# Optimization experiments

Hardware: AMD Instinct MI355X
Metric: run time of the kernel (lower is better)

Reference implementation:

```python
import jax, jax.numpy as jnp
from jax import lax
import numpy as np

MAX_SEQ_LEN = 8192
B, S, D = 8, 8192, 1024
LN_EPS = 1e-5

# ---------- static lattice structure (pure Python, replicates original incl. quirks) ----------

def _gen_spine(max_len):
    s = [0, 2, 4]
    while True:
        nxt = 2 * s[-1] + 2 * s[-2] + 2 * s[-3]
        if nxt >= max_len:
            break
        s.append(nxt)
    return s

def _imm_anc(spine, pos):
    if pos in spine:
        i = spine.index(pos)
        if i >= 3:
            return [spine[i - 1], spine[i - 2], spine[i - 3]]
    return []

def _analyze(spine, pos):
    # BFS over ancestors; NOTE: levels[level+1] is OVERWRITTEN per popped node,
    # exactly as in the original torch code.
    visited = {pos}
    levels = {0: [pos]}
    queue = [(pos, 0)]
    while queue:
        cur, lvl = queue.pop(0)
        if lvl >= 9:
            break
        newl = []
        for a in _imm_anc(spine, cur):
            if a not in visited and a >= 0:
                visited.add(a)
                newl.append(a)
                queue.append((a, lvl + 1))
        if newl:
            levels[lvl + 1] = list(newl)
    max_depth = max(levels.keys())
    pc = {pos: 1}
    for lvl in sorted(levels.keys(), reverse=True):
        for node in levels[lvl]:
            if node == pos:
                continue
            if lvl == max_depth:
                pc[node] = 1
                continue
            c = 0
            for ch in levels.get(lvl + 1, []):
                if node in _imm_anc(spine, ch):
                    c += pc.get(ch, 0)
            if lvl != 0:
                pc[node] = c
    pc.pop(pos, None)
    return levels, pc

def _structures(seq_len):
    spine = _gen_spine(MAX_SEQ_LEN)
    out = []
    for pos in spine:
        if pos >= seq_len or pos < 3:
            continue
        levels, pc = _analyze(spine, pos)
        anc, cnt = [], []
        for lvl in levels:  # dict insertion order == level order, as in torch
            if lvl > 0:
                for a in levels[lvl]:
                    if a < seq_len:
                        anc.append(a)
                        cnt.append(float(pc.get(a, 1)))
        if anc:
            out.append((pos, np.array(anc, np.int32), np.array(cnt, np.float32)))
    return out

# ---------- neural pieces ----------

def _gru_last(seq, w_ih, w_hh, b_ih, b_hh):
    # seq: [B, K, D]; single-layer batch_first GRU, h0 = 0; returns last hidden [B, D]
    d = w_hh.shape[1]
    def step(h, xt):
        gi = xt @ w_ih.T + b_ih   # [B, 3D]
        gh = h @ w_hh.T + b_hh
        i_r, i_z, i_n = jnp.split(gi, 3, axis=-1)
        h_r, h_z, h_n = jnp.split(gh, 3, axis=-1)
        r = jax.nn.sigmoid(i_r + h_r)
        z = jax.nn.sigmoid(i_z + h_z)
        n = jnp.tanh(i_n + r * h_n)
        return (1.0 - z) * n + z * h, None
    h0 = jnp.zeros((seq.shape[0], d), seq.dtype)
    hT, _ = lax.scan(step, h0, jnp.swapaxes(seq, 0, 1))
    return hT

def reference(x, pw_w1, pw_b1, pw_w2, pw_b2, msg_w, msg_b, ln_g, ln_b,
              gru_w_ih, gru_w_hh, gru_b_ih, gru_b_hh, gate_w, gate_b):
    structs = _structures(x.shape[1])
    out = x
    for pos, anc, cnt in structs:
        # path weights: Linear(1,64)->ReLU->Linear(64,1)->Softplus  on counts [K,1]
        c = jnp.asarray(cnt)[:, None]
        w = jax.nn.softplus(jnp.squeeze(jax.nn.relu(c @ pw_w1.T + pw_b1) @ pw_w2.T + pw_b2))  # [K]
        h_anc = x[:, anc, :]                         # [B, K, D] gather
        h_cur = x[:, pos, :]                         # [B, D]
        pair = jnp.concatenate([h_anc, jnp.broadcast_to(h_cur[:, None, :], h_anc.shape)], axis=-1)
        m = pair @ msg_w.T + msg_b                   # [B, K, D]
        mu = m.mean(-1, keepdims=True)
        var = ((m - mu) ** 2).mean(-1, keepdims=True)
        m = (m - mu) / jnp.sqrt(var + LN_EPS) * ln_g + ln_b
        m = jax.nn.gelu(m, approximate=False)
        m = m * w[None, :, None]                     # path-weighted messages
        agg = _gru_last(m, gru_w_ih, gru_w_hh, gru_b_ih, gru_b_hh)  # [B, D]
        g = jax.nn.sigmoid(jnp.concatenate([agg, h_cur], axis=-1) @ gate_w.T + gate_b)
        out = out.at[:, pos, :].set(g * agg + (1.0 - g) * h_cur)
    return out

def setup_inputs() -> dict:
    key = jax.random.key(0)
    ks = jax.random.split(key, 8)
    def n(k, shape, s=0.02):
        return jax.random.normal(k, shape, jnp.float32) * s
    return {
        "x": jax.random.normal(ks[0], (B, S, D), jnp.float32),
        "pw_w1": n(ks[1], (64, 1), 0.5), "pw_b1": jnp.zeros((64,), jnp.float32),
        "pw_w2": n(ks[2], (1, 64), 0.5), "pw_b2": jnp.zeros((1,), jnp.float32),
        "msg_w": n(ks[3], (D, 2 * D)), "msg_b": jnp.zeros((D,), jnp.float32),
        "ln_g": jnp.ones((D,), jnp.float32), "ln_b": jnp.zeros((D,), jnp.float32),
        "gru_w_ih": n(ks[4], (3 * D, D)), "gru_w_hh": n(ks[5], (3 * D, D)),
        "gru_b_ih": jnp.zeros((3 * D,), jnp.float32), "gru_b_hh": jnp.zeros((3 * D,), jnp.float32),
        "gate_w": n(ks[6], (D, 2 * D)), "gate_b": jnp.zeros((D,), jnp.float32),
    }
```

## Files before the change

### kernel.cpp

```cpp
#include <hip/hip_runtime.h>
#include <math.h>
#include <string.h>

#define SEQ 8192
#define DIM 1024
#define NBATCH 8

typedef float vf4 __attribute__((ext_vector_type(4)));

struct SDesc {
  int n, Tmax, totalRows;
  int pos[8], A[8], rowbase[8];
  int anc[8][8];
  float cnt[8][8];
  int nu;
  int upos[16];
  int up_of_s[8];
  int s_of_rr[32], a_of_rr[32], ua_of_rr[32];
};

static SDesc build_structs() {
  SDesc H{};
  int spine[24];
  int ns = 3; spine[0] = 0; spine[1] = 2; spine[2] = 4;
  for (;;) {
    long nxt = 2L * (spine[ns-1] + spine[ns-2] + spine[ns-3]);
    if (nxt >= SEQ) break;
    spine[ns++] = (int)nxt;
  }
  int rb = 0;
  for (int i = 0; i < ns; ++i) {
    int pos = spine[i];
    if (pos < 3) continue;
    bool visited[24] = {false};
    int levels[12][8]; int lcnt[12];
    for (int l = 0; l < 12; ++l) lcnt[l] = 0;
    levels[0][0] = i; lcnt[0] = 1; visited[i] = true;
    int qidx[64], qlvl[64], qh = 0, qt = 0;
    qidx[qt] = i; qlvl[qt] = 0; qt++;
    int maxd = 0;
    while (qh < qt) {
      int cur = qidx[qh], lvl = qlvl[qh]; qh++;
      if (lvl >= 9) break;
      int newl[8], nn = 0;
      if (cur >= 3) {
        for (int d = 1; d <= 3; ++d) {
          int a = cur - d;
          if (!visited[a]) { visited[a] = true; newl[nn++] = a; qidx[qt] = a; qlvl[qt] = lvl + 1; qt++; }
        }
      }
      if (nn) {
        lcnt[lvl+1] = nn;
        for (int k = 0; k < nn; ++k) levels[lvl+1][k] = newl[k];
        if (lvl + 1 > maxd) maxd = lvl + 1;
      }
    }
    float pcv[24]; bool pcs[24];
    for (int k = 0; k < 24; ++k) { pcv[k] = 0.f; pcs[k] = false; }
    pcv[i] = 1.f; pcs[i] = true;
    for (int lvl = maxd; lvl >= 0; --lvl) {
      for (int nidx = 0; nidx < lcnt[lvl]; ++nidx) {
        int node = levels[lvl][nidx];
        if (node == i) continue;
        if (lvl == maxd) { pcv[node] = 1.f; pcs[node] = true; continue; }
        float c = 0.f;
        for (int cidx = 0; cidx < lcnt[lvl+1]; ++cidx) {
          int ch = levels[lvl+1][cidx];
          if (ch >= 3 && node >= ch - 3 && node <= ch - 1) c += pcs[ch] ? pcv[ch] : 0.f;
        }
        if (lvl != 0) { pcv[node] = c; pcs[node] = true; }
      }
    }
    int A = 0;
    int sidx = H.n;
    for (int lvl = 1; lvl <= maxd; ++lvl) {
      for (int nidx = 0; nidx < lcnt[lvl]; ++nidx) {
        int node = levels[lvl][nidx];
        H.anc[sidx][A] = spine[node];
        H.cnt[sidx][A] = pcs[node] ? pcv[node] : 1.f;
        A++;
      }
    }
    if (A == 0) continue;
    H.pos[sidx] = pos; H.A[sidx] = A; H.rowbase[sidx] = rb; rb += A;
    H.n++;
  }
  H.totalRows = rb;
  H.Tmax = 0;
  for (int s = 0; s < H.n; ++s) if (H.A[s] > H.Tmax) H.Tmax = H.A[s];
  int vals[128], nv = 0;
  for (int s = 0; s < H.n; ++s) {
    vals[nv++] = H.pos[s];
    for (int a = 0; a < H.A[s]; ++a) vals[nv++] = H.anc[s][a];
  }
  H.nu = 0;
  for (int i = 0; i < nv; ++i) {
    bool seen = false;
    for (int u = 0; u < H.nu; ++u) if (H.upos[u] == vals[i]) { seen = true; break; }
    if (!seen) H.upos[H.nu++] = vals[i];
  }
  for (int i = 0; i < H.nu; ++i)
    for (int j2 = i + 1; j2 < H.nu; ++j2)
      if (H.upos[j2] < H.upos[i]) { int t = H.upos[i]; H.upos[i] = H.upos[j2]; H.upos[j2] = t; }
  auto uidx = [&](int v) { for (int u = 0; u < H.nu; ++u) if (H.upos[u] == v) return u; return 0; };
  for (int s = 0; s < H.n; ++s) {
    H.up_of_s[s] = uidx(H.pos[s]);
    for (int a = 0; a < H.A[s]; ++a) {
      int rr = H.rowbase[s] + a;
      H.s_of_rr[rr] = s; H.a_of_rr[rr] = a; H.ua_of_rr[rr] = uidx(H.anc[s][a]);
    }
  }
  return H;
}


__device__ __forceinline__ void do_copy(const vf4* __restrict__ src, vf4* __restrict__ dst,
                                        int q, int nc, int start4, int n4) {
  for (int i = q * 256 + threadIdx.x; i < n4; i += nc * 256) {
    vf4 v = __builtin_nontemporal_load(&src[start4 + i]);
    __builtin_nontemporal_store(v, &dst[start4 + i]);
  }
}

__device__ __forceinline__ float wred(float v) {
  #pragma unroll
  for (int off = 32; off; off >>= 1) v += __shfl_xor(v, off);
  return v;
}

__device__ __forceinline__ float dot4(vf4 a, vf4 b) {
  return a.x * b.x + a.y * b.y + a.z * b.z + a.w * b.w;
}


__global__ void k_prepzero(SDesc sd, const float* __restrict__ w1, const float* __restrict__ b1,
                           const float* __restrict__ w2, const float* __restrict__ b2,
                           float* __restrict__ wout, vf4* __restrict__ hz, int nzero4,
                           int NC, const vf4* __restrict__ csrc, vf4* __restrict__ cdst,
                           int cstart, int cn) {
  int p = blockIdx.x;
  if (p >= 57) { do_copy(csrc, cdst, p - 57, NC, cstart, cn); return; }
  if (p == 0) {
    int t = threadIdx.x;
    int s = t >> 3, a = t & 7;
    if (t < 64 && s < sd.n && a < sd.A[s]) {
      float v = sd.cnt[s][a];
      float acc = 0.f;
      for (int i = 0; i < 64; ++i) {
        float h = v * w1[i] + b1[i];
        if (h > 0.f) acc += h * w2[i];
      }
      float o = acc + b2[0];
      float sp = (o > 0.f) ? (o + log1pf(expf(-o))) : log1pf(expf(o));
      wout[s * 8 + a] = sp;
    }
  } else {
    int base = (p - 1) * 512 + threadIdx.x;
    if (base < nzero4)       hz[base]       = (vf4)(0.f);
    if (base + 256 < nzero4) hz[base + 256] = (vf4)(0.f);
  }
}

__global__ __launch_bounds__(256, 2) void k_T(SDesc sd, const float* __restrict__ x,
    const float* __restrict__ msg_w, float* __restrict__ T,
    int NC, const vf4* __restrict__ csrc, vf4* __restrict__ cdst, int cstart, int cn) {
  int p = blockIdx.x;
  const int NMAIN = 1280;
  if (p >= NMAIN) { do_copy(csrc, cdst, p - NMAIN, NC, cstart, cn); return; }
  int q = p % 128, rt = p / 128;
  int jt = (q & 7) * 16 + (q >> 3);

  int wave = threadIdx.x >> 6, lane = threadIdx.x & 63;
  int jc0 = jt * 16 + wave * 4;
  const vf4* mw4 = (const vf4*)msg_w;
  size_t b0 = (size_t)((jc0 + 0) & 1023) * 512 + (((jc0 + 0) >> 10) << 8);
  size_t b1 = (size_t)((jc0 + 1) & 1023) * 512 + (((jc0 + 1) >> 10) << 8);
  size_t b2 = (size_t)((jc0 + 2) & 1023) * 512 + (((jc0 + 2) >> 10) << 8);
  size_t b3 = (size_t)((jc0 + 3) & 1023) * 512 + (((jc0 + 3) >> 10) << 8);
  vf4 w0[4], w1[4], w2[4], w3[4];
  #pragma unroll
  for (int c = 0; c < 4; ++c) {
    w0[c] = mw4[b0 + c * 64 + lane];
    w1[c] = mw4[b1 + c * 64 + lane];
    w2[c] = mw4[b2 + c * 64 + lane];
    w3[c] = mw4[b3 + c * 64 + lane];
  }
  const vf4* x4 = (const vf4*)x;
  #pragma unroll 2
  for (int r = 0; r < 8; ++r) {
    int row = rt * 8 + r; int u = row >> 3, b = row & 7;
    size_t rb4 = ((size_t)b * SEQ + sd.upos[u]) * 256;
    vf4 a0 = x4[rb4 + 0 * 64 + lane], a1 = x4[rb4 + 1 * 64 + lane];
    vf4 a2 = x4[rb4 + 2 * 64 + lane], a3 = x4[rb4 + 3 * 64 + lane];
    float s0 = dot4(w0[0], a0) + dot4(w0[1], a1) + dot4(w0[2], a2) + dot4(w0[3], a3);
    float s1 = dot4(w1[0], a0) + dot4(w1[1], a1) + dot4(w1[2], a2) + dot4(w1[3], a3);
    float s2 = dot4(w2[0], a0) + dot4(w2[1], a1) + dot4(w2[2], a2) + dot4(w2[3], a3);
    float s3 = dot4(w3[0], a0) + dot4(w3[1], a1) + dot4(w3[2], a2) + dot4(w3[3], a3);
    s0 = wred(s0); s1 = wred(s1); s2 = wred(s2); s3 = wred(s3);
    if (lane == 0) {
      float* tp = T + (size_t)row * 2048 + jc0;
      tp[0] = s0; tp[1] = s1; tp[2] = s2; tp[3] = s3;
    }
  }
}

__global__ __launch_bounds__(256) void k_ln(SDesc sd, const float* __restrict__ ln_g,
    const float* __restrict__ ln_b, const float* __restrict__ msg_b,
    const float* __restrict__ wsc, const float* __restrict__ T, float* __restrict__ mseq,
    int M, int NC, const vf4* __restrict__ csrc, vf4* __restrict__ cdst, int cstart, int cn) {
  int p = blockIdx.x;
  if (p >= M) { do_copy(csrc, cdst, p - M, NC, cstart, cn); return; }
  int rr = p >> 3, b = p & 7;
  int s = sd.s_of_rr[rr], a = sd.a_of_rr[rr];
  int ua = sd.ua_of_rr[rr], up = sd.up_of_s[s];
  float wmul = wsc[s * 8 + a];
  const vf4* Tl = (const vf4*)(T + ((size_t)ua * 8 + b) * 2048);
  const vf4* Tr = (const vf4*)(T + ((size_t)up * 8 + b) * 2048 + 1024);
  const vf4* mb = (const vf4*)msg_b;
  int t = threadIdx.x;
  vf4 vl = Tl[t], vr = Tr[t], vb = mb[t];
  vf4 v; v.x = vl.x + vr.x + vb.x; v.y = vl.y + vr.y + vb.y;
  v.z = vl.z + vr.z + vb.z; v.w = vl.w + vr.w + vb.w;
  float sum = v.x + v.y + v.z + v.w;
  float sq  = v.x * v.x + v.y * v.y + v.z * v.z + v.w * v.w;
  #pragma unroll
  for (int off = 32; off; off >>= 1) { sum += __shfl_xor(sum, off); sq += __shfl_xor(sq, off); }
  __shared__ float s1[4], s2[4];
  int wave = t >> 6, lane = t & 63;
  if (lane == 0) { s1[wave] = sum; s2[wave] = sq; }
  __syncthreads();
  sum = s1[0] + s1[1] + s1[2] + s1[3];
  sq  = s2[0] + s2[1] + s2[2] + s2[3];
  float mu  = sum * (1.f / 1024.f);
  float var = sq * (1.f / 1024.f) - mu * mu;
  float inv = rsqrtf(var + 1e-5f);
  vf4 g4 = ((const vf4*)ln_g)[t];
  vf4 b4 = ((const vf4*)ln_b)[t];
  float o[4]  = {v.x, v.y, v.z, v.w};
  float gg[4] = {g4.x, g4.y, g4.z, g4.w};
  float bb[4] = {b4.x, b4.y, b4.z, b4.w};
  #pragma unroll
  for (int i = 0; i < 4; ++i) {
    float u = (o[i] - mu) * inv * gg[i] + bb[i];
    float ge = 0.5f * u * (1.f + erff(u * 0.70710678118654752f));
    o[i] = ge * wmul;
  }
  vf4 ov; ov.x = o[0]; ov.y = o[1]; ov.z = o[2]; ov.w = o[3];
  ((vf4*)(mseq + (size_t)p * DIM))[t] = ov;
}

__global__ __launch_bounds__(256, 2) void k_gi(const float* __restrict__ mseq,
    const float* __restrict__ wih, const float* __restrict__ bih, float* __restrict__ gi,
    int NC, const vf4* __restrict__ csrc, vf4* __restrict__ cdst, int cstart, int cn) {
  int p = blockIdx.x;
  const int NMAIN = 2880;
  if (p >= NMAIN) { do_copy(csrc, cdst, p - NMAIN, NC, cstart, cn); return; }
  int q = p % 192, rt = p / 192;
  int jt = (q & 7) * 24 + (q >> 3);

  int wave = threadIdx.x >> 6, lane = threadIdx.x & 63;
  int j0 = jt * 16 + wave * 4;
  const vf4* wp4 = (const vf4*)wih;
  vf4 w0[4], w1[4], w2[4], w3[4];
  #pragma unroll
  for (int c = 0; c < 4; ++c) {
    w0[c] = wp4[(size_t)(j0 + 0) * 256 + c * 64 + lane];
    w1[c] = wp4[(size_t)(j0 + 1) * 256 + c * 64 + lane];
    w2[c] = wp4[(size_t)(j0 + 2) * 256 + c * 64 + lane];
    w3[c] = wp4[(size_t)(j0 + 3) * 256 + c * 64 + lane];
  }
  const vf4* m4 = (const vf4*)mseq;
  #pragma unroll 2
  for (int r = 0; r < 16; ++r) {
    int row = rt * 16 + r;
    size_t rb4 = (size_t)row * 256;
    vf4 a0 = m4[rb4 + 0 * 64 + lane], a1 = m4[rb4 + 1 * 64 + lane];
    vf4 a2 = m4[rb4 + 2 * 64 + lane], a3 = m4[rb4 + 3 * 64 + lane];
    float s0 = dot4(w0[0], a0) + dot4(w0[1], a1) + dot4(w0[2], a2) + dot4(w0[3], a3);
    float s1 = dot4(w1[0], a0) + dot4(w1[1], a1) + dot4(w1[2], a2) + dot4(w1[3], a3);
    float s2 = dot4(w2[0], a0) + dot4(w2[1], a1) + dot4(w2[2], a2) + dot4(w2[3], a3);
    float s3 = dot4(w3[0], a0) + dot4(w3[1], a1) + dot4(w3[2], a2) + dot4(w3[3], a3);
    s0 = wred(s0); s1 = wred(s1); s2 = wred(s2); s3 = wred(s3);
    if (lane == 0) {
      float* gp = gi + (size_t)row * 3072 + j0;
      gp[0] = s0 + bih[j0 + 0]; gp[1] = s1 + bih[j0 + 1];
      gp[2] = s2 + bih[j0 + 2]; gp[3] = s3 + bih[j0 + 3];
    }
  }
}

__global__ __launch_bounds__(256, 2) void k_step(SDesc sd, int t,
    const float* __restrict__ whh, const float* __restrict__ bhh,
    const float* __restrict__ gi, const float* __restrict__ hold, float* __restrict__ hnew,
    int NC, const vf4* __restrict__ csrc, vf4* __restrict__ cdst, int cstart, int cn) {
  int p = blockIdx.x;
  const int NMAIN = 7 * 256;
  if (p >= NMAIN) { do_copy(csrc, cdst, p - NMAIN, NC, cstart, cn); return; }
  int q = p & 255, s = p >> 8;
  int jt = (q & 7) * 32 + (q >> 3);
  int t0 = sd.Tmax - sd.A[s];
  if (t < t0) return;
  int a = t - t0;

  int wave = threadIdx.x >> 6, lane = threadIdx.x & 63;
  int j = jt * 4 + wave;
  const vf4* wp4 = (const vf4*)whh;
  vf4 wr[4], wz[4], wn[4];
  #pragma unroll
  for (int c = 0; c < 4; ++c) {
    wr[c] = wp4[(size_t)j * 256 + c * 64 + lane];
    wz[c] = wp4[(size_t)(1024 + j) * 256 + c * 64 + lane];
    wn[c] = wp4[(size_t)(2048 + j) * 256 + c * 64 + lane];
  }
  const vf4* h4 = (const vf4*)hold;
  #pragma unroll 2
  for (int r = 0; r < 8; ++r) {
    int srow = s * 8 + r;
    size_t rb4 = (size_t)srow * 256;
    vf4 a0 = h4[rb4 + 0 * 64 + lane], a1 = h4[rb4 + 1 * 64 + lane];
    vf4 a2 = h4[rb4 + 2 * 64 + lane], a3 = h4[rb4 + 3 * 64 + lane];
    float ar = dot4(wr[0], a0) + dot4(wr[1], a1) + dot4(wr[2], a2) + dot4(wr[3], a3);
    float az = dot4(wz[0], a0) + dot4(wz[1], a1) + dot4(wz[2], a2) + dot4(wz[3], a3);
    float an = dot4(wn[0], a0) + dot4(wn[1], a1) + dot4(wn[2], a2) + dot4(wn[3], a3);
    ar = wred(ar); az = wred(az); an = wred(an);
    if (lane == 0) {
      int girow = (sd.rowbase[s] + a) * 8 + r;
      const float* gp = gi + (size_t)girow * 3072;
      float hr = ar + bhh[j];
      float hz = az + bhh[1024 + j];
      float hn = an + bhh[2048 + j];
      float rg = 1.f / (1.f + expf(-(gp[j] + hr)));
      float zg = 1.f / (1.f + expf(-(gp[1024 + j] + hz)));
      float ng = tanhf(gp[2048 + j] + rg * hn);
      float ho = hold[(size_t)srow * DIM + j];
      hnew[(size_t)srow * DIM + j] = (1.f - zg) * ng + zg * ho;
    }
  }
}

__global__ __launch_bounds__(256, 2) void k_gate(SDesc sd, const float* __restrict__ x,
    const float* __restrict__ gw, const float* __restrict__ gb,
    const float* __restrict__ hfin, float* __restrict__ out) {
  int p = blockIdx.x;
  int q = p % 128, rt = p / 128;
  int jt = (q & 7) * 16 + (q >> 3);

  int wave = threadIdx.x >> 6, lane = threadIdx.x & 63;
  int j0 = jt * 8 + wave * 2;
  const vf4* g4p = (const vf4*)gw;
  vf4 wL0[4], wR0[4], wL1[4], wR1[4];
  #pragma unroll
  for (int c = 0; c < 4; ++c) {
    wL0[c] = g4p[(size_t)(j0 + 0) * 512 + c * 64 + lane];
    wR0[c] = g4p[(size_t)(j0 + 0) * 512 + 256 + c * 64 + lane];
    wL1[c] = g4p[(size_t)(j0 + 1) * 512 + c * 64 + lane];
    wR1[c] = g4p[(size_t)(j0 + 1) * 512 + 256 + c * 64 + lane];
  }
  const vf4* h4 = (const vf4*)hfin;
  const vf4* x4 = (const vf4*)x;
  #pragma unroll 2
  for (int r = 0; r < 8; ++r) {
    int row = rt * 8 + r; int s = row >> 3, b = row & 7;
    size_t ab4 = (size_t)row * 256;
    size_t xb4 = ((size_t)b * SEQ + sd.pos[s]) * 256;
    vf4 a0 = h4[ab4 + 0 * 64 + lane], a1 = h4[ab4 + 1 * 64 + lane];
    vf4 a2 = h4[ab4 + 2 * 64 + lane], a3 = h4[ab4 + 3 * 64 + lane];
    vf4 x0 = x4[xb4 + 0 * 64 + lane], x1 = x4[xb4 + 1 * 64 + lane];
    vf4 x2 = x4[xb4 + 2 * 64 + lane], x3 = x4[xb4 + 3 * 64 + lane];
    float s0 = dot4(wL0[0], a0) + dot4(wL0[1], a1) + dot4(wL0[2], a2) + dot4(wL0[3], a3)
             + dot4(wR0[0], x0) + dot4(wR0[1], x1) + dot4(wR0[2], x2) + dot4(wR0[3], x3);
    float s1 = dot4(wL1[0], a0) + dot4(wL1[1], a1) + dot4(wL1[2], a2) + dot4(wL1[3], a3)
             + dot4(wR1[0], x0) + dot4(wR1[1], x1) + dot4(wR1[2], x2) + dot4(wR1[3], x3);
    s0 = wred(s0); s1 = wred(s1);
    if (lane == 0) {
      #pragma unroll
      for (int jj = 0; jj < 2; ++jj) {
        int j = j0 + jj;
        float sv = jj ? s1 : s0;
        float g = 1.f / (1.f + expf(-(sv + gb[j])));
        float agg = hfin[(size_t)row * DIM + j];
        float hc  = x[((size_t)b * SEQ + sd.pos[s]) * DIM + j];
        out[((size_t)b * SEQ + sd.pos[s]) * DIM + j] = g * agg + (1.f - g) * hc;
      }
    }
  }
}


extern "C" void kernel_launch(void* const* d_in, const int* in_sizes, int n_in,
                              void* d_out, int out_size, void* d_ws, size_t ws_size,
                              hipStream_t stream) {
  const float* x      = (const float*)d_in[0];
  const float* pw_w1  = (const float*)d_in[1];
  const float* pw_b1  = (const float*)d_in[2];
  const float* pw_w2  = (const float*)d_in[3];
  const float* pw_b2  = (const float*)d_in[4];
  const float* msg_w  = (const float*)d_in[5];
  const float* msg_b  = (const float*)d_in[6];
  const float* ln_g   = (const float*)d_in[7];
  const float* ln_b   = (const float*)d_in[8];
  const float* w_ih   = (const float*)d_in[9];
  const float* w_hh   = (const float*)d_in[10];
  const float* b_ih   = (const float*)d_in[11];
  const float* b_hh   = (const float*)d_in[12];
  const float* gate_w = (const float*)d_in[13];
  const float* gate_b = (const float*)d_in[14];
  float* out = (float*)d_out;
  float* ws  = (float*)d_ws;

  SDesc sd = build_structs();
  const int M = sd.totalRows * 8;

  float* wout = ws;
  float* T    = wout + 64;
  float* mseq = T + (size_t)sd.nu * 8 * 2048;
  float* gi   = mseq + (size_t)240 * DIM;
  float* h0   = gi + (size_t)240 * 3072;
  float* h1   = h0 + (size_t)sd.n * 8 * DIM;

  const vf4* x4 = (const vf4*)x;
  vf4* out4 = (vf4*)out;
  const int TOTAL4 = (NBATCH * SEQ * DIM) / 4;
  const int c_big = 2200000;
  const int rem = TOTAL4 - 4 * c_big;
  const int c_step = rem / 5;

  int nzero4 = (2 * sd.n * 8 * DIM) / 4;

  int off = 0;
  k_prepzero<<<57 + 1024, 256, 0, stream>>>(sd, pw_w1, pw_b1, pw_w2, pw_b2, wout,
                                            (vf4*)h0, nzero4, 1024, x4, out4, off, c_big);
  off += c_big;

  k_T<<<1280 + 1024, 256, 0, stream>>>(sd, x, msg_w, T, 1024, x4, out4, off, c_big);
  off += c_big;

  k_ln<<<M + 1024, 256, 0, stream>>>(sd, ln_g, ln_b, msg_b, wout, T, mseq,
                                     M, 1024, x4, out4, off, c_big);
  off += c_big;

  k_gi<<<2880 + 1024, 256, 0, stream>>>(mseq, w_ih, b_ih, gi, 1024, x4, out4, off, c_big);
  off += c_big;

  for (int t = 0; t < sd.Tmax; ++t) {
    const float* hr = (t & 1) ? h1 : h0;
    float*       hw = (t & 1) ? h0 : h1;
    int cnt = (t == sd.Tmax - 1) ? (TOTAL4 - off) : c_step;
    k_step<<<7 * 256 + 768, 256, 0, stream>>>(sd, t, w_hh, b_hh, gi, hr, hw,
                                              768, x4, out4, off, cnt);
    off += cnt;
  }
  const float* hfin = (sd.Tmax & 1) ? h1 : h0;

  k_gate<<<128 * 7, 256, 0, stream>>>(sd, x, gate_w, gate_b, hfin, out);

  (void)in_sizes; (void)n_in; (void)out_size; (void)ws_size;
}
```

Measured before the change: 301.5 us.

## Skip hidden-state zeroing by special-casing first GRU step, fuse prep into k_T

Removes the separate prep/zero kernel. The pathweight MLP now runs as an extra block inside k_T, and the first GRU step (a==0) computes its result directly with h=0, so there is no zeroed h buffer to read and no W_hh matvec for that step. The step kernel hoists the gi and bias loads out of the lane-0 epilogue, occupancy hints rise from 2 to 4 blocks per CU, and the background copy is split into new per-kernel chunk sizes with more copy blocks. This saves a launch and some memory traffic, but higher occupancy may force register spills in the weight-resident kernels.

```diff
diff --git a/kernel.cpp b/kernel.cpp
--- a/kernel.cpp
+++ b/kernel.cpp
@@ -133,14 +133,14 @@
 }
 
 
-__global__ void k_prepzero(SDesc sd, const float* __restrict__ w1, const float* __restrict__ b1,
-                           const float* __restrict__ w2, const float* __restrict__ b2,
-                           float* __restrict__ wout, vf4* __restrict__ hz, int nzero4,
-                           int NC, const vf4* __restrict__ csrc, vf4* __restrict__ cdst,
-                           int cstart, int cn) {
+__global__ __launch_bounds__(256, 4) void k_T(SDesc sd, const float* __restrict__ x,
+    const float* __restrict__ msg_w, float* __restrict__ T,
+    const float* __restrict__ w1, const float* __restrict__ b1,
+    const float* __restrict__ w2, const float* __restrict__ b2, float* __restrict__ wout,
+    int NC, const vf4* __restrict__ csrc, vf4* __restrict__ cdst, int cstart, int cn) {
   int p = blockIdx.x;
-  if (p >= 57) { do_copy(csrc, cdst, p - 57, NC, cstart, cn); return; }
-  if (p == 0) {
+  const int NMAIN = 1280;
+  if (p == NMAIN) {
     int t = threadIdx.x;
     int s = t >> 3, a = t & 7;
     if (t < 64 && s < sd.n && a < sd.A[s]) {
@@ -154,19 +154,9 @@
       float sp = (o > 0.f) ? (o + log1pf(expf(-o))) : log1pf(expf(o));
       wout[s * 8 + a] = sp;
     }
-  } else {
-    int base = (p - 1) * 512 + threadIdx.x;
-    if (base < nzero4)       hz[base]       = (vf4)(0.f);
-    if (base + 256 < nzero4) hz[base + 256] = (vf4)(0.f);
-  }
-}
-
-__global__ __launch_bounds__(256, 2) void k_T(SDesc sd, const float* __restrict__ x,
-    const float* __restrict__ msg_w, float* __restrict__ T,
-    int NC, const vf4* __restrict__ csrc, vf4* __restrict__ cdst, int cstart, int cn) {
-  int p = blockIdx.x;
-  const int NMAIN = 1280;
-  if (p >= NMAIN) { do_copy(csrc, cdst, p - NMAIN, NC, cstart, cn); return; }
+    return;
+  }
+  if (p > NMAIN) { do_copy(csrc, cdst, p - NMAIN - 1, NC, cstart, cn); return; }
   int q = p % 128, rt = p / 128;
   int jt = (q & 7) * 16 + (q >> 3);
 
@@ -174,16 +164,16 @@
   int jc0 = jt * 16 + wave * 4;
   const vf4* mw4 = (const vf4*)msg_w;
   size_t b0 = (size_t)((jc0 + 0) & 1023) * 512 + (((jc0 + 0) >> 10) << 8);
-  size_t b1 = (size_t)((jc0 + 1) & 1023) * 512 + (((jc0 + 1) >> 10) << 8);
-  size_t b2 = (size_t)((jc0 + 2) & 1023) * 512 + (((jc0 + 2) >> 10) << 8);
+  size_t b1_ = (size_t)((jc0 + 1) & 1023) * 512 + (((jc0 + 1) >> 10) << 8);
+  size_t b2_ = (size_t)((jc0 + 2) & 1023) * 512 + (((jc0 + 2) >> 10) << 8);
   size_t b3 = (size_t)((jc0 + 3) & 1023) * 512 + (((jc0 + 3) >> 10) << 8);
-  vf4 w0[4], w1[4], w2[4], w3[4];
+  vf4 w0[4], w1v[4], w2v[4], w3[4];
   #pragma unroll
   for (int c = 0; c < 4; ++c) {
-    w0[c] = mw4[b0 + c * 64 + lane];
-    w1[c] = mw4[b1 + c * 64 + lane];
-    w2[c] = mw4[b2 + c * 64 + lane];
-    w3[c] = mw4[b3 + c * 64 + lane];
+    w0[c]  = mw4[b0  + c * 64 + lane];
+    w1v[c] = mw4[b1_ + c * 64 + lane];
+    w2v[c] = mw4[b2_ + c * 64 + lane];
+    w3[c]  = mw4[b3  + c * 64 + lane];
   }
   const vf4* x4 = (const vf4*)x;
   #pragma unroll 2
@@ -192,10 +182,10 @@
     size_t rb4 = ((size_t)b * SEQ + sd.upos[u]) * 256;
     vf4 a0 = x4[rb4 + 0 * 64 + lane], a1 = x4[rb4 + 1 * 64 + lane];
     vf4 a2 = x4[rb4 + 2 * 64 + lane], a3 = x4[rb4 + 3 * 64 + lane];
-    float s0 = dot4(w0[0], a0) + dot4(w0[1], a1) + dot4(w0[2], a2) + dot4(w0[3], a3);
-    float s1 = dot4(w1[0], a0) + dot4(w1[1], a1) + dot4(w1[2], a2) + dot4(w1[3], a3);
-    float s2 = dot4(w2[0], a0) + dot4(w2[1], a1) + dot4(w2[2], a2) + dot4(w2[3], a3);
-    float s3 = dot4(w3[0], a0) + dot4(w3[1], a1) + dot4(w3[2], a2) + dot4(w3[3], a3);
+    float s0 = dot4(w0[0],  a0) + dot4(w0[1],  a1) + dot4(w0[2],  a2) + dot4(w0[3],  a3);
+    float s1 = dot4(w1v[0], a0) + dot4(w1v[1], a1) + dot4(w1v[2], a2) + dot4(w1v[3], a3);
+    float s2 = dot4(w2v[0], a0) + dot4(w2v[1], a1) + dot4(w2v[2], a2) + dot4(w2v[3], a3);
+    float s3 = dot4(w3[0],  a0) + dot4(w3[1],  a1) + dot4(w3[2],  a2) + dot4(w3[3],  a3);
     s0 = wred(s0); s1 = wred(s1); s2 = wred(s2); s3 = wred(s3);
     if (lane == 0) {
       float* tp = T + (size_t)row * 2048 + jc0;
@@ -249,7 +239,7 @@
   ((vf4*)(mseq + (size_t)p * DIM))[t] = ov;
 }
 
-__global__ __launch_bounds__(256, 2) void k_gi(const float* __restrict__ mseq,
+__global__ __launch_bounds__(256, 4) void k_gi(const float* __restrict__ mseq,
     const float* __restrict__ wih, const float* __restrict__ bih, float* __restrict__ gi,
     int NC, const vf4* __restrict__ csrc, vf4* __restrict__ cdst, int cstart, int cn) {
   int p = blockIdx.x;
@@ -289,7 +279,7 @@
   }
 }
 
-__global__ __launch_bounds__(256, 2) void k_step(SDesc sd, int t,
+__global__ __launch_bounds__(256, 4) void k_step(SDesc sd, int t,
     const float* __restrict__ whh, const float* __restrict__ bhh,
     const float* __restrict__ gi, const float* __restrict__ hold, float* __restrict__ hnew,
     int NC, const vf4* __restrict__ csrc, vf4* __restrict__ cdst, int cstart, int cn) {
@@ -304,6 +294,20 @@
 
   int wave = threadIdx.x >> 6, lane = threadIdx.x & 63;
   int j = jt * 4 + wave;
+  int girow0 = (sd.rowbase[s] + a) * 8;
+
+  if (a == 0) {
+    if (lane < 8) {
+      int r = lane;
+      const float* gp = gi + (size_t)(girow0 + r) * 3072;
+      float rg = 1.f / (1.f + expf(-(gp[j] + bhh[j])));
+      float zg = 1.f / (1.f + expf(-(gp[1024 + j] + bhh[1024 + j])));
+      float ng = tanhf(gp[2048 + j] + rg * bhh[2048 + j]);
+      hnew[(size_t)(s * 8 + r) * DIM + j] = (1.f - zg) * ng;
+    }
+    return;
+  }
+
   const vf4* wp4 = (const vf4*)whh;
   vf4 wr[4], wz[4], wn[4];
   #pragma unroll
@@ -312,11 +316,14 @@
     wz[c] = wp4[(size_t)(1024 + j) * 256 + c * 64 + lane];
     wn[c] = wp4[(size_t)(2048 + j) * 256 + c * 64 + lane];
   }
+  float bj_r = bhh[j], bj_z = bhh[1024 + j], bj_n = bhh[2048 + j];
   const vf4* h4 = (const vf4*)hold;
   #pragma unroll 2
   for (int r = 0; r < 8; ++r) {
     int srow = s * 8 + r;
     size_t rb4 = (size_t)srow * 256;
+    const float* gp = gi + (size_t)(girow0 + r) * 3072;
+    float gir = gp[j], giz = gp[1024 + j], gin = gp[2048 + j];
     vf4 a0 = h4[rb4 + 0 * 64 + lane], a1 = h4[rb4 + 1 * 64 + lane];
     vf4 a2 = h4[rb4 + 2 * 64 + lane], a3 = h4[rb4 + 3 * 64 + lane];
     float ar = dot4(wr[0], a0) + dot4(wr[1], a1) + dot4(wr[2], a2) + dot4(wr[3], a3);
@@ -324,21 +331,16 @@
     float an = dot4(wn[0], a0) + dot4(wn[1], a1) + dot4(wn[2], a2) + dot4(wn[3], a3);
     ar = wred(ar); az = wred(az); an = wred(an);
     if (lane == 0) {
-      int girow = (sd.rowbase[s] + a) * 8 + r;
-      const float* gp = gi + (size_t)girow * 3072;
-      float hr = ar + bhh[j];
-      float hz = az + bhh[1024 + j];
-      float hn = an + bhh[2048 + j];
-      float rg = 1.f / (1.f + expf(-(gp[j] + hr)));
-      float zg = 1.f / (1.f + expf(-(gp[1024 + j] + hz)));
-      float ng = tanhf(gp[2048 + j] + rg * hn);
+      float rg = 1.f / (1.f + expf(-(gir + ar + bj_r)));
+      float zg = 1.f / (1.f + expf(-(giz + az + bj_z)));
+      float ng = tanhf(gin + rg * (an + bj_n));
       float ho = hold[(size_t)srow * DIM + j];
       hnew[(size_t)srow * DIM + j] = (1.f - zg) * ng + zg * ho;
     }
   }
 }
 
-__global__ __launch_bounds__(256, 2) void k_gate(SDesc sd, const float* __restrict__ x,
+__global__ __launch_bounds__(256, 4) void k_gate(SDesc sd, const float* __restrict__ x,
     const float* __restrict__ gw, const float* __restrict__ gb,
     const float* __restrict__ hfin, float* __restrict__ out) {
   int p = blockIdx.x;
@@ -421,33 +423,32 @@
   const vf4* x4 = (const vf4*)x;
   vf4* out4 = (vf4*)out;
   const int TOTAL4 = (NBATCH * SEQ * DIM) / 4;
-  const int c_big = 2200000;
-  const int rem = TOTAL4 - 4 * c_big;
-  const int c_step = rem / 5;
-
-  int nzero4 = (2 * sd.n * 8 * DIM) / 4;
+
+  const int c_T  = 2200000;
+  const int c_ln = 2400000;
+  const int c_gi = 1800000;
+  const int c_s0 = 2600000;
+  const int c_s  = 1900000;
 
   int off = 0;
-  k_prepzero<<<57 + 1024, 256, 0, stream>>>(sd, pw_w1, pw_b1, pw_w2, pw_b2, wout,
-                                            (vf4*)h0, nzero4, 1024, x4, out4, off, c_big);
-  off += c_big;
-
-  k_T<<<1280 + 1024, 256, 0, stream>>>(sd, x, msg_w, T, 1024, x4, out4, off, c_big);
-  off += c_big;
-
-  k_ln<<<M + 1024, 256, 0, stream>>>(sd, ln_g, ln_b, msg_b, wout, T, mseq,
-                                     M, 1024, x4, out4, off, c_big);
-  off += c_big;
-
-  k_gi<<<2880 + 1024, 256, 0, stream>>>(mseq, w_ih, b_ih, gi, 1024, x4, out4, off, c_big);
-  off += c_big;
+  k_T<<<1280 + 1 + 1024, 256, 0, stream>>>(sd, x, msg_w, T,
+                                           pw_w1, pw_b1, pw_w2, pw_b2, wout,
+                                           1024, x4, out4, off, c_T);
+  off += c_T;
+
+  k_ln<<<M + 1280, 256, 0, stream>>>(sd, ln_g, ln_b, msg_b, wout, T, mseq,
+                                     M, 1280, x4, out4, off, c_ln);
+  off += c_ln;
+
+  k_gi<<<2880 + 1024, 256, 0, stream>>>(mseq, w_ih, b_ih, gi, 1024, x4, out4, off, c_gi);
+  off += c_gi;
 
   for (int t = 0; t < sd.Tmax; ++t) {
     const float* hr = (t & 1) ? h1 : h0;
     float*       hw = (t & 1) ? h0 : h1;
-    int cnt = (t == sd.Tmax - 1) ? (TOTAL4 - off) : c_step;
-    k_step<<<7 * 256 + 768, 256, 0, stream>>>(sd, t, w_hh, b_hh, gi, hr, hw,
-                                              768, x4, out4, off, cnt);
+    int cnt = (t == 0) ? c_s0 : (t == sd.Tmax - 1) ? (TOTAL4 - off) : c_s;
+    k_step<<<7 * 256 + 1280, 256, 0, stream>>>(sd, t, w_hh, b_hh, gi, hr, hw,
+                                               1280, x4, out4, off, cnt);
     off += cnt;
   }
   const float* hfin = (sd.Tmax & 1) ? h1 : h0;
```

Result: faster. 266.1 us (-11.7%).
